# Performance work log

Hardware: AMD Instinct MI355X
Metric: run time of the kernel (lower is better)

## Reference

```python
import jax, jax.numpy as jnp
import numpy as np

L, H, P = 16384, 256, 512


def setup_inputs() -> dict:
    key = jax.random.key(0)
    ks = jax.random.split(key, 7)
    return {
        "input_sequence": jax.random.normal(ks[0], (L, H), jnp.float32),
        "A_diag": jax.random.normal(ks[1], (P,), jnp.float32) * 2.0,
        "G_diag": jax.random.uniform(ks[2], (P,), jnp.float32),  # in [0,1): keeps 1 - sigmoid(dt)*G > 0
        "dt": jax.random.normal(ks[3], (P,), jnp.float32) * 0.5,
        "B": jax.random.uniform(ks[4], (P, H, 2), jnp.float32, -1.0, 1.0) / np.sqrt(H).astype(np.float32),
        "C": jax.random.uniform(ks[5], (H, P, 2), jnp.float32, -1.0, 1.0) / np.sqrt(P).astype(np.float32),
        "D": jax.random.normal(ks[6], (H,), jnp.float32),
    }


def _combine(q_i, q_j):
    # q = (A, b); A: (..., 4, P) real 2x2 block-diagonal entries [A,B,C,D], b: (..., 2, P) complex
    A_i, b_i = q_i
    A_j, b_j = q_j
    iA, iB, iC, iD = A_i[..., 0, :], A_i[..., 1, :], A_i[..., 2, :], A_i[..., 3, :]
    jA, jB, jC, jD = A_j[..., 0, :], A_j[..., 1, :], A_j[..., 2, :], A_j[..., 3, :]
    A_new = jnp.stack(
        [jA * iA + jB * iC, jA * iB + jB * iD, jC * iA + jD * iC, jC * iB + jD * iD],
        axis=-2,
    )
    b1, b2 = b_i[..., 0, :], b_i[..., 1, :]
    b_new = jnp.stack([jA * b1 + jB * b2, jC * b1 + jD * b2], axis=-2) + b_j
    return (A_new, b_new)


def reference(input_sequence, A_diag, G_diag, dt, B, C, D):
    # complex parameter assembly
    B_c = B[..., 0] + 1j * B[..., 1]      # (P, H) complex
    C_c = C[..., 0] + 1j * C[..., 1]      # (H, P) complex

    # _soft_project_AGdt
    dts = jax.nn.sigmoid(dt)
    G = jax.nn.relu(G_diag)
    root = jnp.sqrt(1.0 - dts * G)
    denom = jnp.maximum(dts ** 2, 1e-6)
    A_low = (2.0 - dts * G - 2.0 * root) / denom
    A_high = (2.0 - dts * G + 2.0 * root) / denom
    A = A_low + jax.nn.relu(A_diag - A_low) - jax.nn.relu(A_diag - A_high)

    # Bu_k = B_complex @ u_k for all k: (L, P) complex64
    Bu = input_sequence.astype(B_c.dtype) @ B_c.T

    # IMEX2 transition matrix (diagonal 2x2 blocks), constant over time
    M = jnp.stack(
        [1.0 - dts * G, -dts * A, dts * (1.0 - dts * G), 1.0 - dts ** 2 * A],
        axis=0,
    )  # (4, P)
    seq_len = input_sequence.shape[0]
    M_el = jnp.broadcast_to(M, (seq_len, 4, M.shape[-1]))          # (L, 4, P)
    F = jnp.stack([dts * Bu, dts ** 2 * Bu], axis=1)               # (L, 2, P) complex

    _, xs = jax.lax.associative_scan(_combine, (M_el, F))
    ys = xs[:, 1, :]                                                # x-component, (L, P) complex

    out = (ys @ C_c.T).real.astype(input_sequence.dtype) + input_sequence * D
    return out
```

## Files before the change

### kernel.cpp

```cpp
#include <hip/hip_runtime.h>
#include <math.h>

#define L_SEQ 16384
#define H_DIM 256
#define P_DIM 512
#define CL 32
#define NC (L_SEQ / CL)

typedef __attribute__((ext_vector_type(8))) short bf16x8;
typedef __attribute__((ext_vector_type(4))) float f32x4;

static __device__ __forceinline__ unsigned short f2bf(float f) {
  unsigned int u = __builtin_bit_cast(unsigned int, f);
  u += 0x7FFFu + ((u >> 16) & 1u);
  return (unsigned short)(u >> 16);
}
static __device__ __forceinline__ float bflo(unsigned int v) {
  return __builtin_bit_cast(float, v << 16);
}
static __device__ __forceinline__ float bfhi(unsigned int v) {
  return __builtin_bit_cast(float, v & 0xFFFF0000u);
}
static __device__ __forceinline__ float bf2f(unsigned short s) {
  return __builtin_bit_cast(float, (unsigned int)s << 16);
}
static __device__ __forceinline__ unsigned int pack2(float r, float i) {
  return (unsigned int)f2bf(r) | ((unsigned int)f2bf(i) << 16);
}

__global__ __launch_bounds__(256) void prep_all(
    const float* __restrict__ A_diag, const float* __restrict__ G_diag,
    const float* __restrict__ dt, const float* __restrict__ B,
    const float* __restrict__ C, const float* __restrict__ u,
    float* __restrict__ prm, unsigned short* __restrict__ W1b,
    unsigned short* __restrict__ W2b, unsigned short* __restrict__ ub,
    float* __restrict__ aT, float* __restrict__ bT) {
  const int b = blockIdx.x;
  const int t = threadIdx.x;
  if (b < 2) {
    int p = b * 256 + t;
    float dts = 1.0f / (1.0f + expf(-dt[p]));
    float G = fmaxf(G_diag[p], 0.0f);
    float g = dts * G;
    float root = sqrtf(1.0f - g);
    float denom = fmaxf(dts * dts, 1e-6f);
    float A_low  = (2.0f - g - 2.0f * root) / denom;
    float A_high = (2.0f - g + 2.0f * root) / denom;
    float Ad = A_diag[p];
    float A = A_low + fmaxf(Ad - A_low, 0.0f) - fmaxf(Ad - A_high, 0.0f);
    float m00 = 1.0f - g;
    float m01 = -dts * A;
    float m10 = dts * (1.0f - g);
    float m11 = 1.0f - dts * dts * A;
    float e00 = m00, e01 = m01, e10 = m10, e11 = m11;
    for (int s = 0; s < 32; s++) {
      aT[s * P_DIM + p] = e10;
      bT[s * P_DIM + p] = e11;
      float f00 = m00 * e00 + m01 * e10;
      float f01 = m00 * e01 + m01 * e11;
      float f10 = m10 * e00 + m11 * e10;
      float f11 = m10 * e01 + m11 * e11;
      e00 = f00; e01 = f01; e10 = f10; e11 = f11;
    }
    float c00 = m00, c01 = m01, c10 = m10, c11 = m11;
#pragma unroll
    for (int i = 0; i < 5; i++) {
      float n00 = c00 * c00 + c01 * c10;
      float n01 = c00 * c01 + c01 * c11;
      float n10 = c10 * c00 + c11 * c10;
      float n11 = c10 * c01 + c11 * c11;
      c00 = n00; c01 = n01; c10 = n10; c11 = n11;
    }
    prm[0 * P_DIM + p] = m00;
    prm[1 * P_DIM + p] = m01;
    prm[2 * P_DIM + p] = m10;
    prm[3 * P_DIM + p] = m11;
    prm[4 * P_DIM + p] = dts;
    prm[5 * P_DIM + p] = dts * dts;
    prm[6 * P_DIM + p] = c00;
    prm[7 * P_DIM + p] = c01;
    prm[8 * P_DIM + p] = c10;
    prm[9 * P_DIM + p] = c11;
  } else if (b < 2 + 1024) {
    int idx = (b - 2) * 256 + t;
    int n = idx >> 8;
    int k = idx & 255;
    int p = n >> 1, c = n & 1;
    W1b[((size_t)(k >> 3) * 1024 + n) * 8 + (k & 7)] = f2bf(B[(p * H_DIM + k) * 2 + c]);
  } else if (b < 2 + 2048) {
    int idx = (b - 1026) * 256 + t;
    int h = idx >> 10;
    int k = idx & 1023;
    int p = k >> 1, c = k & 1;
    float v = C[(h * P_DIM + p) * 2 + c];
    W2b[((size_t)(k >> 3) * 256 + h) * 8 + (k & 7)] = f2bf(c ? -v : v);
  } else {
    int idx = (b - 2050) * 256 + t;
    float4 v = ((const float4*)u)[idx];
    ushort4 o;
    o.x = f2bf(v.x); o.y = f2bf(v.y); o.z = f2bf(v.z); o.w = f2bf(v.w);
    ((ushort4*)ub)[idx] = o;
  }
}

__global__ __launch_bounds__(256) void gemm1_scan(
    const unsigned short* __restrict__ A, const unsigned short* __restrict__ W,
    unsigned int* __restrict__ ys,
    const float* __restrict__ prm, float4* __restrict__ finals) {
  constexpr int K = H_DIM;
  __shared__ unsigned short tA[128 * 32];
  __shared__ unsigned short tW[128 * 32];
  __shared__ unsigned short stg[128 * 132];
  const int tid = threadIdx.x;
  const int lane = tid & 63;
  const int wid = tid >> 6;
  const int wr = wid >> 1;
  const int wc = wid & 1;
  const int bm = blockIdx.x * 128;
  const int bn = blockIdx.y * 128;

  f32x4 acc[4][4] = {};
  const int rA = lane & 15;
  const int g = lane >> 4;

  for (int k0 = 0; k0 < K; k0 += 32) {
    __syncthreads();
#pragma unroll
    for (int c = wid; c < 8; c += 4) {
      const int unit = c * 64 + lane;
      const int kg = unit >> 7, r = unit & 127;
      const unsigned short* src = A + ((size_t)(bm + r) * 32 + (k0 >> 3) + kg) * 8;
      __builtin_amdgcn_global_load_lds(
          (const __attribute__((address_space(1))) void*)src,
          (__attribute__((address_space(3))) void*)(tA + c * 512), 16, 0, 0);
    }
#pragma unroll
    for (int c = wid; c < 8; c += 4) {
      const int unit = c * 64 + lane;
      const int kg = unit >> 7, n = unit & 127;
      const unsigned short* src = W + ((size_t)((k0 >> 3) + kg) * 1024 + bn + n) * 8;
      __builtin_amdgcn_global_load_lds(
          (const __attribute__((address_space(1))) void*)src,
          (__attribute__((address_space(3))) void*)(tW + c * 512), 16, 0, 0);
    }
    __syncthreads();

    bf16x8 af[4], wf[4];
#pragma unroll
    for (int i = 0; i < 4; i++)
      af[i] = *(const bf16x8*)&tA[(g * 128 + wr * 64 + i * 16 + rA) * 8];
#pragma unroll
    for (int j = 0; j < 4; j++)
      wf[j] = *(const bf16x8*)&tW[(g * 128 + wc * 64 + j * 16 + rA) * 8];
#pragma unroll
    for (int i = 0; i < 4; i++)
#pragma unroll
      for (int j = 0; j < 4; j++)
        acc[i][j] = __builtin_amdgcn_mfma_f32_16x16x32_bf16(af[i], wf[j], acc[i][j], 0, 0, 0);
  }

  const int cr = (lane >> 4) * 4;
  const int cc = lane & 15;
#pragma unroll
  for (int i = 0; i < 4; i++)
#pragma unroll
    for (int j = 0; j < 4; j++) {
      const int rl = wr * 64 + i * 16 + cr;
      const int clc = wc * 64 + j * 16 + cc;
#pragma unroll
      for (int q = 0; q < 4; q++)
        stg[(rl + q) * 132 + clc] = f2bf(acc[i][j][q]);
    }

  __syncthreads();
  {
    const int i = tid >> 6;
    const int pl = tid & 63;
    const int p = (bn >> 1) + pl;
    const int cglob = blockIdx.x * 4 + i;
    float m00 = prm[0 * P_DIM + p], m01 = prm[1 * P_DIM + p];
    float m10 = prm[2 * P_DIM + p], m11 = prm[3 * P_DIM + p];
    float dts = prm[4 * P_DIM + p], dts2 = prm[5 * P_DIM + p];
    float x1r = 0.f, x2r = 0.f, x1i = 0.f, x2i = 0.f;
    const unsigned int* stg32 = (const unsigned int*)stg;
    unsigned int* dst = ys + (size_t)(bm + i * 32) * P_DIM + p;
#pragma unroll 8
    for (int s = 0; s < CL; s++) {
      unsigned int v = stg32[(i * 32 + s) * 66 + pl];
      float bx = bflo(v), by = bfhi(v);
      float n1r = fmaf(m00, x1r, fmaf(m01, x2r, dts * bx));
      float n2r = fmaf(m10, x1r, fmaf(m11, x2r, dts2 * bx));
      float n1i = fmaf(m00, x1i, fmaf(m01, x2i, dts * by));
      float n2i = fmaf(m10, x1i, fmaf(m11, x2i, dts2 * by));
      dst[(size_t)s * P_DIM] = pack2(n2r, n2i);
      x1r = n1r; x2r = n2r; x1i = n1i; x2i = n2i;
    }
    finals[(size_t)cglob * P_DIM + p] = make_float4(x1r, x2r, x1i, x2i);
  }
}

__global__ __launch_bounds__(NC) void scan_carry(
    const float4* __restrict__ finals, const float* __restrict__ prm,
    float4* __restrict__ carry) {
  int p = blockIdx.x;
  int c = threadIdx.x;
  __shared__ float4 sb[NC];
  float m00 = prm[6 * P_DIM + p], m01 = prm[7 * P_DIM + p];
  float m10 = prm[8 * P_DIM + p], m11 = prm[9 * P_DIM + p];
  float4 b = finals[c * P_DIM + p];
  for (int o = 1; o < NC; o <<= 1) {
    sb[c] = b;
    __syncthreads();
    float4 nb = (c >= o) ? sb[c - o] : make_float4(0.f, 0.f, 0.f, 0.f);
    __syncthreads();
    b.x = fmaf(m00, nb.x, fmaf(m01, nb.y, b.x));
    b.y = fmaf(m10, nb.x, fmaf(m11, nb.y, b.y));
    b.z = fmaf(m00, nb.z, fmaf(m01, nb.w, b.z));
    b.w = fmaf(m10, nb.z, fmaf(m11, nb.w, b.w));
    float n00 = m00 * m00 + m01 * m10;
    float n01 = m00 * m01 + m01 * m11;
    float n10 = m10 * m00 + m11 * m10;
    float n11 = m10 * m01 + m11 * m11;
    m00 = n00; m01 = n01; m10 = n10; m11 = n11;
  }
  if (c + 1 < NC) carry[(c + 1) * P_DIM + p] = b;
  if (c == 0) carry[p] = make_float4(0.f, 0.f, 0.f, 0.f);
}

__global__ __launch_bounds__(256) void correct_ys(
    unsigned int* __restrict__ ys, const float4* __restrict__ carry,
    const float* __restrict__ aT, const float* __restrict__ bT) {
  const int i4 = blockIdx.x * 256 + threadIdx.x;
  const int tg = i4 >> 7;
  const int p0 = (i4 & 127) * 4;
  const int c = tg >> 5, t = tg & 31;
  uint4 v = ((const uint4*)ys)[i4];
  const float4 a = *(const float4*)&aT[t * P_DIM + p0];
  const float4 b = *(const float4*)&bT[t * P_DIM + p0];
  const float4* cb = carry + (size_t)c * P_DIM + p0;
  float4 x0 = cb[0], x1 = cb[1], x2 = cb[2], x3 = cb[3];
  v.x = pack2(bflo(v.x) + a.x * x0.x + b.x * x0.y, bfhi(v.x) + a.x * x0.z + b.x * x0.w);
  v.y = pack2(bflo(v.y) + a.y * x1.x + b.y * x1.y, bfhi(v.y) + a.y * x1.z + b.y * x1.w);
  v.z = pack2(bflo(v.z) + a.z * x2.x + b.z * x2.y, bfhi(v.z) + a.z * x2.z + b.z * x2.w);
  v.w = pack2(bflo(v.w) + a.w * x3.x + b.w * x3.y, bfhi(v.w) + a.w * x3.z + b.w * x3.w);
  ((uint4*)ys)[i4] = v;
}

__global__ __launch_bounds__(256) void gemm2_lean(
    const unsigned short* __restrict__ ys16, const unsigned short* __restrict__ W2b,
    const unsigned short* __restrict__ ub, const float* __restrict__ Dv,
    float* __restrict__ out) {
  __shared__ unsigned short tA[2][64 * 32];
  __shared__ unsigned short tW[2][128 * 32];
  const int tid = threadIdx.x;
  const int lane = tid & 63;
  const int wid = tid >> 6;
  const int bm = blockIdx.x * 64;
  const int bn = blockIdx.y * 128;

  const int rA = lane & 15;
  const int g = lane >> 4;
  const int wr = wid >> 1;
  const int wc = wid & 1;

  const int a_row = (wid * 64 + lane) >> 2;
  const int a_sd = (wid * 64 + lane) & 3;
  const int a_ss = a_sd ^ ((a_row >> 1) & 3);

  auto STAGE = [&](int buf, int k0) {
    {
      const unsigned short* src = ys16 + (size_t)(bm + a_row) * 1024 + k0 + a_ss * 8;
      __builtin_amdgcn_global_load_lds(
          (const __attribute__((address_space(1))) void*)src,
          (__attribute__((address_space(3))) void*)(&tA[buf][wid * 512]), 16, 0, 0);
    }
#pragma unroll
    for (int c = wid; c < 8; c += 4) {
      const int unit = c * 64 + lane;
      const int kg = unit >> 7, n = unit & 127;
      const unsigned short* src = W2b + (((size_t)(k0 >> 3) + kg) * 256 + bn + n) * 8;
      __builtin_amdgcn_global_load_lds(
          (const __attribute__((address_space(1))) void*)src,
          (__attribute__((address_space(3))) void*)(&tW[buf][c * 512]), 16, 0, 0);
    }
  };

  f32x4 acc[2][4] = {};
  STAGE(0, 0);
  __syncthreads();

  for (int t = 0; t < 32; t++) {
    const int cur = t & 1;
    if (t < 31) STAGE(cur ^ 1, (t + 1) * 32);
    bf16x8 af[2], wf[4];
#pragma unroll
    for (int m = 0; m < 2; m++) {
      const int r = wr * 32 + m * 16 + rA;
      const int unit = r * 4 + (g ^ ((r >> 1) & 3));
      af[m] = *(const bf16x8*)&tA[cur][unit * 8];
    }
#pragma unroll
    for (int j = 0; j < 4; j++)
      wf[j] = *(const bf16x8*)&tW[cur][(g * 128 + wc * 64 + j * 16 + rA) * 8];
#pragma unroll
    for (int m = 0; m < 2; m++)
#pragma unroll
      for (int j = 0; j < 4; j++)
        acc[m][j] = __builtin_amdgcn_mfma_f32_16x16x32_bf16(af[m], wf[j], acc[m][j], 0, 0, 0);
    __syncthreads();
  }

  const int cr = (lane >> 4) * 4;
  const int cc = lane & 15;
#pragma unroll
  for (int m = 0; m < 2; m++)
#pragma unroll
    for (int j = 0; j < 4; j++) {
      const int rowg = bm + wr * 32 + m * 16 + cr;
      const int col = bn + wc * 64 + j * 16 + cc;
      const float d = Dv[col];
#pragma unroll
      for (int q = 0; q < 4; q++) {
        const size_t idx = (size_t)(rowg + q) * H_DIM + col;
        out[idx] = fmaf(bf2f(ub[idx]), d, acc[m][j][q]);
      }
    }
}

extern "C" void kernel_launch(void* const* d_in, const int* in_sizes, int n_in,
                              void* d_out, int out_size, void* d_ws, size_t ws_size,
                              hipStream_t stream) {
  const float* u      = (const float*)d_in[0];
  const float* A_diag = (const float*)d_in[1];
  const float* G_diag = (const float*)d_in[2];
  const float* dt     = (const float*)d_in[3];
  const float* B      = (const float*)d_in[4];
  const float* C      = (const float*)d_in[5];
  const float* D      = (const float*)d_in[6];
  float* out = (float*)d_out;

  char* w = (char*)d_ws;
  unsigned short* ys16 = (unsigned short*)w;
  unsigned short* ub   = (unsigned short*)(w + (size_t)L_SEQ * 1024 * 2);
  unsigned short* W1b  = ub + (size_t)L_SEQ * H_DIM;
  unsigned short* W2b  = W1b + 1024 * H_DIM;
  float* prm    = (float*)(W2b + H_DIM * 1024);
  float* finals = prm + 8192;
  float* carryb = finals + (size_t)NC * P_DIM * 4;
  float* aT     = carryb + (size_t)NC * P_DIM * 4;
  float* bT     = aT + 32 * P_DIM;

  prep_all<<<2 + 1024 + 1024 + 4096, 256, 0, stream>>>(
      A_diag, G_diag, dt, B, C, u, prm, W1b, W2b, ub, aT, bT);

  gemm1_scan<<<dim3(L_SEQ / 128, 1024 / 128), 256, 0, stream>>>(
      ub, W1b, (unsigned int*)ys16, prm, (float4*)finals);

  scan_carry<<<P_DIM, NC, 0, stream>>>(
      (const float4*)finals, prm, (float4*)carryb);

  correct_ys<<<(L_SEQ * P_DIM / 4) / 256, 256, 0, stream>>>(
      (unsigned int*)ys16, (const float4*)carryb, aT, bT);

  gemm2_lean<<<dim3(L_SEQ / 64, H_DIM / 128), 256, 0, stream>>>(
      ys16, W2b, ub, D, out);
}
```

Before: 88.24 us.

## Fuse GEMM1, chunked scan, carry, correction and GEMM2 into one cooperative kernel

Replaces the four post-prep kernels with a single cooperative kernel of 256 blocks, one per 64-row chunk. Each block keeps its bf16 ys chunk resident in 128 KB of swizzled LDS through the local scan, grid-synced carry scan, correction and the output GEMM. This removes the global round trip of the large ys intermediate and three launch boundaries. The cost is that the GEMMs now read operands straight from global memory with no LDS staging, occupancy is one block per CU, and the design depends on two grid-wide syncs and the chunk size doubling to 64.

Measured after the change: 126.3 us. 1.43x slower.

```diff
diff --git a/kernel.cpp b/kernel.cpp
--- a/kernel.cpp
+++ b/kernel.cpp
@@ -1,10 +1,13 @@
 #include <hip/hip_runtime.h>
+#include <hip/hip_cooperative_groups.h>
 #include <math.h>
+
+namespace cg = cooperative_groups;
 
 #define L_SEQ 16384
 #define H_DIM 256
 #define P_DIM 512
-#define CL 32
+#define CL 64
 #define NC (L_SEQ / CL)
 
 typedef __attribute__((ext_vector_type(8))) short bf16x8;
@@ -26,6 +29,11 @@
 }
 static __device__ __forceinline__ unsigned int pack2(float r, float i) {
   return (unsigned int)f2bf(r) | ((unsigned int)f2bf(i) << 16);
+}
+static __device__ __forceinline__ int swz_n(int row, int n) {
+  int seg = n >> 3;
+  seg = (seg & 0x70) | ((seg ^ row) & 0x0F);
+  return seg * 8 + (n & 7);
 }
 
 __global__ __launch_bounds__(256) void prep_all(
@@ -53,7 +61,7 @@
     float m10 = dts * (1.0f - g);
     float m11 = 1.0f - dts * dts * A;
     float e00 = m00, e01 = m01, e10 = m10, e11 = m11;
-    for (int s = 0; s < 32; s++) {
+    for (int s = 0; s < 64; s++) {
       aT[s * P_DIM + p] = e10;
       bT[s * P_DIM + p] = e11;
       float f00 = m00 * e00 + m01 * e10;
@@ -64,7 +72,7 @@
     }
     float c00 = m00, c01 = m01, c10 = m10, c11 = m11;
 #pragma unroll
-    for (int i = 0; i < 5; i++) {
+    for (int i = 0; i < 6; i++) {
       float n00 = c00 * c00 + c01 * c10;
       float n01 = c00 * c01 + c01 * c11;
       float n10 = c10 * c00 + c11 * c10;
@@ -103,228 +111,159 @@
   }
 }
 
-__global__ __launch_bounds__(256) void gemm1_scan(
-    const unsigned short* __restrict__ A, const unsigned short* __restrict__ W,
-    unsigned int* __restrict__ ys,
-    const float* __restrict__ prm, float4* __restrict__ finals) {
-  constexpr int K = H_DIM;
-  __shared__ unsigned short tA[128 * 32];
-  __shared__ unsigned short tW[128 * 32];
-  __shared__ unsigned short stg[128 * 132];
+__global__ __launch_bounds__(512) void mega(
+    const unsigned short* __restrict__ ub, const unsigned short* __restrict__ W1b,
+    const unsigned short* __restrict__ W2b, const float* __restrict__ prm,
+    const float* __restrict__ aT, const float* __restrict__ bT,
+    const float* __restrict__ Dv, float4* __restrict__ finals,
+    float4* __restrict__ carry, float* __restrict__ out) {
+  extern __shared__ char smem[];
+  unsigned short* ysl = (unsigned short*)smem;
+  float4* sb = (float4*)(smem + 131072);
+
+  cg::grid_group grid = cg::this_grid();
   const int tid = threadIdx.x;
   const int lane = tid & 63;
   const int wid = tid >> 6;
-  const int wr = wid >> 1;
-  const int wc = wid & 1;
-  const int bm = blockIdx.x * 128;
-  const int bn = blockIdx.y * 128;
-
-  f32x4 acc[4][4] = {};
+  const int blk = blockIdx.x;
+  const int bm = blk * 64;
   const int rA = lane & 15;
-  const int g = lane >> 4;
-
-  for (int k0 = 0; k0 < K; k0 += 32) {
-    __syncthreads();
-#pragma unroll
-    for (int c = wid; c < 8; c += 4) {
-      const int unit = c * 64 + lane;
-      const int kg = unit >> 7, r = unit & 127;
-      const unsigned short* src = A + ((size_t)(bm + r) * 32 + (k0 >> 3) + kg) * 8;
-      __builtin_amdgcn_global_load_lds(
-          (const __attribute__((address_space(1))) void*)src,
-          (__attribute__((address_space(3))) void*)(tA + c * 512), 16, 0, 0);
-    }
-#pragma unroll
-    for (int c = wid; c < 8; c += 4) {
-      const int unit = c * 64 + lane;
-      const int kg = unit >> 7, n = unit & 127;
-      const unsigned short* src = W + ((size_t)((k0 >> 3) + kg) * 1024 + bn + n) * 8;
-      __builtin_amdgcn_global_load_lds(
-          (const __attribute__((address_space(1))) void*)src,
-          (__attribute__((address_space(3))) void*)(tW + c * 512), 16, 0, 0);
-    }
-    __syncthreads();
-
-    bf16x8 af[4], wf[4];
-#pragma unroll
-    for (int i = 0; i < 4; i++)
-      af[i] = *(const bf16x8*)&tA[(g * 128 + wr * 64 + i * 16 + rA) * 8];
-#pragma unroll
-    for (int j = 0; j < 4; j++)
-      wf[j] = *(const bf16x8*)&tW[(g * 128 + wc * 64 + j * 16 + rA) * 8];
-#pragma unroll
-    for (int i = 0; i < 4; i++)
-#pragma unroll
-      for (int j = 0; j < 4; j++)
-        acc[i][j] = __builtin_amdgcn_mfma_f32_16x16x32_bf16(af[i], wf[j], acc[i][j], 0, 0, 0);
-  }
-
-  const int cr = (lane >> 4) * 4;
-  const int cc = lane & 15;
-#pragma unroll
-  for (int i = 0; i < 4; i++)
-#pragma unroll
-    for (int j = 0; j < 4; j++) {
-      const int rl = wr * 64 + i * 16 + cr;
-      const int clc = wc * 64 + j * 16 + cc;
-#pragma unroll
-      for (int q = 0; q < 4; q++)
-        stg[(rl + q) * 132 + clc] = f2bf(acc[i][j][q]);
-    }
-
+  const int g  = lane >> 4;
+  const int wr = wid & 1;
+  const int wq = wid >> 1;
+  const int cr = g * 4;
+  const int cc = rA;
+
+  for (int nch = 0; nch < 4; nch++) {
+    const int nc0 = nch * 256 + wq * 64;
+    f32x4 acc[2][4] = {};
+    for (int k0 = 0; k0 < 256; k0 += 32) {
+      bf16x8 af[2], wf[4];
+#pragma unroll
+      for (int m = 0; m < 2; m++) {
+        const int row = bm + wr * 32 + m * 16 + rA;
+        af[m] = *(const bf16x8*)&ub[(size_t)row * 256 + k0 + g * 8];
+      }
+#pragma unroll
+      for (int j = 0; j < 4; j++) {
+        const int n = nc0 + j * 16 + rA;
+        wf[j] = *(const bf16x8*)&W1b[(((size_t)(k0 >> 3) + g) * 1024 + n) * 8];
+      }
+#pragma unroll
+      for (int m = 0; m < 2; m++)
+#pragma unroll
+        for (int j = 0; j < 4; j++)
+          acc[m][j] = __builtin_amdgcn_mfma_f32_16x16x32_bf16(af[m], wf[j], acc[m][j], 0, 0, 0);
+    }
+#pragma unroll
+    for (int m = 0; m < 2; m++)
+#pragma unroll
+      for (int j = 0; j < 4; j++) {
+        const int rl = wr * 32 + m * 16 + cr;
+        const int n = nc0 + j * 16 + cc;
+#pragma unroll
+        for (int q = 0; q < 4; q++)
+          ysl[(rl + q) * 1024 + swz_n(rl + q, n)] = f2bf(acc[m][j][q]);
+      }
+  }
   __syncthreads();
+
   {
-    const int i = tid >> 6;
-    const int pl = tid & 63;
-    const int p = (bn >> 1) + pl;
-    const int cglob = blockIdx.x * 4 + i;
+    const int p = tid;
     float m00 = prm[0 * P_DIM + p], m01 = prm[1 * P_DIM + p];
     float m10 = prm[2 * P_DIM + p], m11 = prm[3 * P_DIM + p];
     float dts = prm[4 * P_DIM + p], dts2 = prm[5 * P_DIM + p];
     float x1r = 0.f, x2r = 0.f, x1i = 0.f, x2i = 0.f;
-    const unsigned int* stg32 = (const unsigned int*)stg;
-    unsigned int* dst = ys + (size_t)(bm + i * 32) * P_DIM + p;
-#pragma unroll 8
-    for (int s = 0; s < CL; s++) {
-      unsigned int v = stg32[(i * 32 + s) * 66 + pl];
+    for (int row = 0; row < 64; row++) {
+      unsigned int* addr = (unsigned int*)&ysl[row * 1024 + swz_n(row, 2 * p)];
+      unsigned int v = *addr;
       float bx = bflo(v), by = bfhi(v);
       float n1r = fmaf(m00, x1r, fmaf(m01, x2r, dts * bx));
       float n2r = fmaf(m10, x1r, fmaf(m11, x2r, dts2 * bx));
       float n1i = fmaf(m00, x1i, fmaf(m01, x2i, dts * by));
       float n2i = fmaf(m10, x1i, fmaf(m11, x2i, dts2 * by));
-      dst[(size_t)s * P_DIM] = pack2(n2r, n2i);
+      *addr = pack2(n2r, n2i);
       x1r = n1r; x2r = n2r; x1i = n1i; x2i = n2i;
     }
-    finals[(size_t)cglob * P_DIM + p] = make_float4(x1r, x2r, x1i, x2i);
-  }
-}
-
-__global__ __launch_bounds__(NC) void scan_carry(
-    const float4* __restrict__ finals, const float* __restrict__ prm,
-    float4* __restrict__ carry) {
-  int p = blockIdx.x;
-  int c = threadIdx.x;
-  __shared__ float4 sb[NC];
-  float m00 = prm[6 * P_DIM + p], m01 = prm[7 * P_DIM + p];
-  float m10 = prm[8 * P_DIM + p], m11 = prm[9 * P_DIM + p];
-  float4 b = finals[c * P_DIM + p];
-  for (int o = 1; o < NC; o <<= 1) {
-    sb[c] = b;
-    __syncthreads();
-    float4 nb = (c >= o) ? sb[c - o] : make_float4(0.f, 0.f, 0.f, 0.f);
-    __syncthreads();
-    b.x = fmaf(m00, nb.x, fmaf(m01, nb.y, b.x));
-    b.y = fmaf(m10, nb.x, fmaf(m11, nb.y, b.y));
-    b.z = fmaf(m00, nb.z, fmaf(m01, nb.w, b.z));
-    b.w = fmaf(m10, nb.z, fmaf(m11, nb.w, b.w));
-    float n00 = m00 * m00 + m01 * m10;
-    float n01 = m00 * m01 + m01 * m11;
-    float n10 = m10 * m00 + m11 * m10;
-    float n11 = m10 * m01 + m11 * m11;
-    m00 = n00; m01 = n01; m10 = n10; m11 = n11;
-  }
-  if (c + 1 < NC) carry[(c + 1) * P_DIM + p] = b;
-  if (c == 0) carry[p] = make_float4(0.f, 0.f, 0.f, 0.f);
-}
-
-__global__ __launch_bounds__(256) void correct_ys(
-    unsigned int* __restrict__ ys, const float4* __restrict__ carry,
-    const float* __restrict__ aT, const float* __restrict__ bT) {
-  const int i4 = blockIdx.x * 256 + threadIdx.x;
-  const int tg = i4 >> 7;
-  const int p0 = (i4 & 127) * 4;
-  const int c = tg >> 5, t = tg & 31;
-  uint4 v = ((const uint4*)ys)[i4];
-  const float4 a = *(const float4*)&aT[t * P_DIM + p0];
-  const float4 b = *(const float4*)&bT[t * P_DIM + p0];
-  const float4* cb = carry + (size_t)c * P_DIM + p0;
-  float4 x0 = cb[0], x1 = cb[1], x2 = cb[2], x3 = cb[3];
-  v.x = pack2(bflo(v.x) + a.x * x0.x + b.x * x0.y, bfhi(v.x) + a.x * x0.z + b.x * x0.w);
-  v.y = pack2(bflo(v.y) + a.y * x1.x + b.y * x1.y, bfhi(v.y) + a.y * x1.z + b.y * x1.w);
-  v.z = pack2(bflo(v.z) + a.z * x2.x + b.z * x2.y, bfhi(v.z) + a.z * x2.z + b.z * x2.w);
-  v.w = pack2(bflo(v.w) + a.w * x3.x + b.w * x3.y, bfhi(v.w) + a.w * x3.z + b.w * x3.w);
-  ((uint4*)ys)[i4] = v;
-}
-
-__global__ __launch_bounds__(256) void gemm2_lean(
-    const unsigned short* __restrict__ ys16, const unsigned short* __restrict__ W2b,
-    const unsigned short* __restrict__ ub, const float* __restrict__ Dv,
-    float* __restrict__ out) {
-  __shared__ unsigned short tA[2][64 * 32];
-  __shared__ unsigned short tW[2][128 * 32];
-  const int tid = threadIdx.x;
-  const int lane = tid & 63;
-  const int wid = tid >> 6;
-  const int bm = blockIdx.x * 64;
-  const int bn = blockIdx.y * 128;
-
-  const int rA = lane & 15;
-  const int g = lane >> 4;
-  const int wr = wid >> 1;
-  const int wc = wid & 1;
-
-  const int a_row = (wid * 64 + lane) >> 2;
-  const int a_sd = (wid * 64 + lane) & 3;
-  const int a_ss = a_sd ^ ((a_row >> 1) & 3);
-
-  auto STAGE = [&](int buf, int k0) {
-    {
-      const unsigned short* src = ys16 + (size_t)(bm + a_row) * 1024 + k0 + a_ss * 8;
-      __builtin_amdgcn_global_load_lds(
-          (const __attribute__((address_space(1))) void*)src,
-          (__attribute__((address_space(3))) void*)(&tA[buf][wid * 512]), 16, 0, 0);
-    }
-#pragma unroll
-    for (int c = wid; c < 8; c += 4) {
-      const int unit = c * 64 + lane;
-      const int kg = unit >> 7, n = unit & 127;
-      const unsigned short* src = W2b + (((size_t)(k0 >> 3) + kg) * 256 + bn + n) * 8;
-      __builtin_amdgcn_global_load_lds(
-          (const __attribute__((address_space(1))) void*)src,
-          (__attribute__((address_space(3))) void*)(&tW[buf][c * 512]), 16, 0, 0);
-    }
-  };
-
-  f32x4 acc[2][4] = {};
-  STAGE(0, 0);
+    finals[(size_t)blk * P_DIM + p] = make_float4(x1r, x2r, x1i, x2i);
+  }
+  grid.sync();
+
+  {
+    const int pp = tid >> 8;
+    const int c = tid & 255;
+    const int p = blk * 2 + pp;
+    float m00 = prm[6 * P_DIM + p], m01 = prm[7 * P_DIM + p];
+    float m10 = prm[8 * P_DIM + p], m11 = prm[9 * P_DIM + p];
+    float4 b4 = finals[(size_t)c * P_DIM + p];
+    float4* sbp = sb + pp * 256;
+    for (int o = 1; o < NC; o <<= 1) {
+      sbp[c] = b4;
+      __syncthreads();
+      float4 nb = (c >= o) ? sbp[c - o] : make_float4(0.f, 0.f, 0.f, 0.f);
+      __syncthreads();
+      b4.x = fmaf(m00, nb.x, fmaf(m01, nb.y, b4.x));
+      b4.y = fmaf(m10, nb.x, fmaf(m11, nb.y, b4.y));
+      b4.z = fmaf(m00, nb.z, fmaf(m01, nb.w, b4.z));
+      b4.w = fmaf(m10, nb.z, fmaf(m11, nb.w, b4.w));
+      float n00 = m00 * m00 + m01 * m10;
+      float n01 = m00 * m01 + m01 * m11;
+      float n10 = m10 * m00 + m11 * m10;
+      float n11 = m10 * m01 + m11 * m11;
+      m00 = n00; m01 = n01; m10 = n10; m11 = n11;
+    }
+    if (c + 1 < NC) carry[(size_t)(c + 1) * P_DIM + p] = b4;
+    if (c == 0) carry[p] = make_float4(0.f, 0.f, 0.f, 0.f);
+  }
+  grid.sync();
+
+  {
+    const int p = tid;
+    float4 x = carry[(size_t)blk * P_DIM + p];
+    for (int row = 0; row < 64; row++) {
+      float a = aT[row * P_DIM + p];
+      float b = bT[row * P_DIM + p];
+      unsigned int* addr = (unsigned int*)&ysl[row * 1024 + swz_n(row, 2 * p)];
+      unsigned int v = *addr;
+      *addr = pack2(bflo(v) + a * x.x + b * x.y, bfhi(v) + a * x.z + b * x.w);
+    }
+  }
   __syncthreads();
 
-  for (int t = 0; t < 32; t++) {
-    const int cur = t & 1;
-    if (t < 31) STAGE(cur ^ 1, (t + 1) * 32);
-    bf16x8 af[2], wf[4];
-#pragma unroll
-    for (int m = 0; m < 2; m++) {
-      const int r = wr * 32 + m * 16 + rA;
-      const int unit = r * 4 + (g ^ ((r >> 1) & 3));
-      af[m] = *(const bf16x8*)&tA[cur][unit * 8];
-    }
-#pragma unroll
-    for (int j = 0; j < 4; j++)
-      wf[j] = *(const bf16x8*)&tW[cur][(g * 128 + wc * 64 + j * 16 + rA) * 8];
+  {
+    f32x4 acc[2][4] = {};
+    for (int k0 = 0; k0 < 1024; k0 += 32) {
+      bf16x8 af[2], wf[4];
+#pragma unroll
+      for (int m = 0; m < 2; m++) {
+        const int row = wr * 32 + m * 16 + rA;
+        af[m] = *(const bf16x8*)&ysl[row * 1024 + swz_n(row, k0 + g * 8)];
+      }
+#pragma unroll
+      for (int j = 0; j < 4; j++) {
+        const int col = wq * 64 + j * 16 + rA;
+        wf[j] = *(const bf16x8*)&W2b[(((size_t)(k0 >> 3) + g) * 256 + col) * 8];
+      }
+#pragma unroll
+      for (int m = 0; m < 2; m++)
+#pragma unroll
+        for (int j = 0; j < 4; j++)
+          acc[m][j] = __builtin_amdgcn_mfma_f32_16x16x32_bf16(af[m], wf[j], acc[m][j], 0, 0, 0);
+    }
 #pragma unroll
     for (int m = 0; m < 2; m++)
 #pragma unroll
-      for (int j = 0; j < 4; j++)
-        acc[m][j] = __builtin_amdgcn_mfma_f32_16x16x32_bf16(af[m], wf[j], acc[m][j], 0, 0, 0);
-    __syncthreads();
-  }
-
-  const int cr = (lane >> 4) * 4;
-  const int cc = lane & 15;
-#pragma unroll
-  for (int m = 0; m < 2; m++)
-#pragma unroll
-    for (int j = 0; j < 4; j++) {
-      const int rowg = bm + wr * 32 + m * 16 + cr;
-      const int col = bn + wc * 64 + j * 16 + cc;
-      const float d = Dv[col];
-#pragma unroll
-      for (int q = 0; q < 4; q++) {
-        const size_t idx = (size_t)(rowg + q) * H_DIM + col;
-        out[idx] = fmaf(bf2f(ub[idx]), d, acc[m][j][q]);
-      }
-    }
+      for (int j = 0; j < 4; j++) {
+        const int col = wq * 64 + j * 16 + cc;
+        const float d = Dv[col];
+#pragma unroll
+        for (int q = 0; q < 4; q++) {
+          const int row = bm + wr * 32 + m * 16 + cr + q;
+          const size_t idx = (size_t)row * H_DIM + col;
+          out[idx] = fmaf(bf2f(ub[idx]), d, acc[m][j][q]);
+        }
+      }
+  }
 }
 
 extern "C" void kernel_launch(void* const* d_in, const int* in_sizes, int n_in,
@@ -340,28 +279,22 @@
   float* out = (float*)d_out;
 
   char* w = (char*)d_ws;
-  unsigned short* ys16 = (unsigned short*)w;
-  unsigned short* ub   = (unsigned short*)(w + (size_t)L_SEQ * 1024 * 2);
-  unsigned short* W1b  = ub + (size_t)L_SEQ * H_DIM;
-  unsigned short* W2b  = W1b + 1024 * H_DIM;
+  unsigned short* ub  = (unsigned short*)w;
+  unsigned short* W1b = ub + (size_t)L_SEQ * H_DIM;
+  unsigned short* W2b = W1b + 1024 * H_DIM;
   float* prm    = (float*)(W2b + H_DIM * 1024);
   float* finals = prm + 8192;
   float* carryb = finals + (size_t)NC * P_DIM * 4;
   float* aT     = carryb + (size_t)NC * P_DIM * 4;
-  float* bT     = aT + 32 * P_DIM;
+  float* bT     = aT + 64 * P_DIM;
 
   prep_all<<<2 + 1024 + 1024 + 4096, 256, 0, stream>>>(
       A_diag, G_diag, dt, B, C, u, prm, W1b, W2b, ub, aT, bT);
 
-  gemm1_scan<<<dim3(L_SEQ / 128, 1024 / 128), 256, 0, stream>>>(
-      ub, W1b, (unsigned int*)ys16, prm, (float4*)finals);
-
-  scan_carry<<<P_DIM, NC, 0, stream>>>(
-      (const float4*)finals, prm, (float4*)carryb);
-
-  correct_ys<<<(L_SEQ * P_DIM / 4) / 256, 256, 0, stream>>>(
-      (unsigned int*)ys16, (const float4*)carryb, aT, bT);
-
-  gemm2_lean<<<dim3(L_SEQ / 64, H_DIM / 128), 256, 0, stream>>>(
-      ys16, W2b, ub, D, out);
-}
+  void* args[] = {
+      (void*)&ub, (void*)&W1b, (void*)&W2b, (void*)&prm,
+      (void*)&aT, (void*)&bT, (void*)&D, (void*)&finals,
+      (void*)&carryb, (void*)&out};
+  hipLaunchCooperativeKernel((const void*)mega, dim3(NC), dim3(512), args,
+                             131072 + 8192, stream);
+}
```
